# Optimization experiments

Hardware: AMD Instinct MI355X
Metric: run time of the kernel (lower is better)

## Reference

```python
import jax, jax.numpy as jnp
import numpy as np
import math

B, H, S, D = 2, 8, 2048, 64

def setup_inputs() -> dict:
    key = jax.random.key(0)
    kq, kk, kv = jax.random.split(key, 3)
    q = jax.random.normal(kq, (B, H, S, D), dtype=jnp.float32)
    k = jax.random.normal(kk, (B, H, S, D), dtype=jnp.float32)
    v = jax.random.normal(kv, (B, H, S, D), dtype=jnp.float32)
    # causal mask: True means masked (filled with -1e9), matching masked_fill
    mask = jnp.triu(jnp.ones((S, S), dtype=jnp.bool_), k=1)
    return {"q": q, "k": k, "v": v, "mask": mask}

def reference(q, k, v, mask) -> jnp.ndarray:
    d_model = q.shape[-1]
    # [..., s, t] scores
    att = jnp.einsum('bhsd,bhtd->bhst', q, k) / math.sqrt(d_model)
    if mask is not None:
        # broadcast mask over leading dims; True -> -1e9
        att = jnp.where(mask, jnp.float32(-1e9), att)
    # numerically stable softmax over last axis (matches manual Softmax)
    att = jax.nn.softmax(att, axis=-1)
    return jnp.einsum('bhst,bhtd->bhsd', att, v)
```

## Files before the change

kernel.cpp:

```cpp
#include <hip/hip_runtime.h>

typedef __bf16 bf16x8 __attribute__((ext_vector_type(8)));
typedef float  f32x16 __attribute__((ext_vector_type(16)));

constexpr int Sn  = 2048;
constexpr int Dh  = 64;
constexpr int QT  = 32;
constexpr int KVT = 32;
constexpr int NBH = 16;
constexpr int NT  = Sn / QT;
constexpr int NW  = 8;
constexpr int TSTR = 4 * 64 * 8;

constexpr float SCL = 0.125f * 1.44269504088896340736f;

constexpr size_t ELEMS  = (size_t)NBH * Sn * Dh;
constexpr size_t QB_OFF = 0;
constexpr size_t KP_OFF = ELEMS;
constexpr size_t VP_OFF = 2 * ELEMS;
constexpr size_t WS_NEED = 3 * ELEMS * 2;

__device__ inline bf16x8 cvt8(float4 a, float4 b, float s) {
  bf16x8 r;
  r[0] = (__bf16)(a.x * s); r[1] = (__bf16)(a.y * s);
  r[2] = (__bf16)(a.z * s); r[3] = (__bf16)(a.w * s);
  r[4] = (__bf16)(b.x * s); r[5] = (__bf16)(b.y * s);
  r[6] = (__bf16)(b.z * s); r[7] = (__bf16)(b.w * s);
  return r;
}

__global__ __launch_bounds__(256) void prep(
    const float* __restrict__ q, const float* __restrict__ k,
    const float* __restrict__ v, __bf16* __restrict__ ws)
{
  __shared__ float tl[KVT][Dh + 1];
  const int g    = blockIdx.x;
  const int tid  = threadIdx.x;
  const int wv   = tid >> 6;
  const int lane = tid & 63;
  const int hi   = lane >> 5;
  const int ln   = lane & 31;
  const size_t tbase = (size_t)g * (KVT * Dh);

  {
    const float* qp = q + tbase + (size_t)tid * 8;
    const float4 a = *(const float4*)qp;
    const float4 b = *(const float4*)(qp + 4);
    *(bf16x8*)(ws + QB_OFF + tbase + (size_t)tid * 8) = cvt8(a, b, SCL);
  }
  {
    const float* kp = k + tbase;
#pragma unroll
    for (int e = 0; e < 2; ++e) {
      const int i4  = tid + e * 256;
      const float4 x = *(const float4*)(kp + (size_t)i4 * 4);
      const int row = i4 >> 4, col = (i4 & 15) * 4;
      tl[row][col] = x.x; tl[row][col + 1] = x.y;
      tl[row][col + 2] = x.z; tl[row][col + 3] = x.w;
    }
  }
  __syncthreads();
  {
    bf16x8 r;
#pragma unroll
    for (int i = 0; i < 8; ++i) r[i] = (__bf16)tl[ln][16 * wv + 8 * hi + i];
    *(bf16x8*)(ws + KP_OFF + ((size_t)(g * 4 + wv) * 64 + lane) * 8) = r;
  }
  __syncthreads();
  {
    const float* vp = v + tbase;
#pragma unroll
    for (int e = 0; e < 2; ++e) {
      const int i4  = tid + e * 256;
      const float4 x = *(const float4*)(vp + (size_t)i4 * 4);
      const int row = i4 >> 4, col = (i4 & 15) * 4;
      tl[row][col] = x.x; tl[row][col + 1] = x.y;
      tl[row][col + 2] = x.z; tl[row][col + 3] = x.w;
    }
  }
  __syncthreads();
  {
    const int dt = wv >> 1, T = wv & 1;
    bf16x8 r;
#pragma unroll
    for (int i = 0; i < 8; ++i) {
      const int row = 16 * T + 4 * hi + (i & 3) + 8 * (i >> 2);
      r[i] = (__bf16)tl[row][32 * dt + ln];
    }
    *(bf16x8*)(ws + VP_OFF + ((size_t)(g * 4 + wv) * 64 + lane) * 8) = r;
  }
}

#define LOADKV(K0,K1,K2,K3,V0,V1,V2,V3,kt_) do {                         \
    const __bf16* kp_ = kpB + (size_t)(kt_) * TSTR + lane * 8;           \
    K0 = *(const bf16x8*)(kp_);                                          \
    K1 = *(const bf16x8*)(kp_ + 512);                                    \
    K2 = *(const bf16x8*)(kp_ + 1024);                                   \
    K3 = *(const bf16x8*)(kp_ + 1536);                                   \
    const __bf16* vp_ = vpB + (size_t)(kt_) * TSTR + lane * 8;           \
    V0 = *(const bf16x8*)(vp_);                                          \
    V1 = *(const bf16x8*)(vp_ + 512);                                    \
    V2 = *(const bf16x8*)(vp_ + 1024);                                   \
    V3 = *(const bf16x8*)(vp_ + 1536);                                   \
  } while (0)

#define COMPUTE(K0,K1,K2,K3,V0,V1,V2,V3,kt_) do {                        \
    f32x16 st0, st1;                                                     \
    _Pragma("unroll")                                                    \
    for (int i_ = 0; i_ < 16; ++i_) { st0[i_] = 0.f; st1[i_] = 0.f; }    \
    st0 = __builtin_amdgcn_mfma_f32_32x32x16_bf16(K0, qf[0], st0, 0, 0, 0);\
    st1 = __builtin_amdgcn_mfma_f32_32x32x16_bf16(K2, qf[2], st1, 0, 0, 0);\
    st0 = __builtin_amdgcn_mfma_f32_32x32x16_bf16(K1, qf[1], st0, 0, 0, 0);\
    st1 = __builtin_amdgcn_mfma_f32_32x32x16_bf16(K3, qf[3], st1, 0, 0, 0);\
    _Pragma("unroll")                                                    \
    for (int i_ = 0; i_ < 16; ++i_) st0[i_] += st1[i_];                  \
    if ((kt_) == tile) {                                                 \
      _Pragma("unroll")                                                  \
      for (int r_ = 0; r_ < 16; ++r_) {                                  \
        const int tl_ = (r_ & 3) + 8 * (r_ >> 2) + 4 * hi;               \
        if (tl_ > ln) st0[r_] = -1e30f;                                  \
      }                                                                  \
    }                                                                    \
    float p[16];                                                         \
    _Pragma("unroll")                                                    \
    for (int r_ = 0; r_ < 16; ++r_) p[r_] = __builtin_amdgcn_exp2f(st0[r_]); \
    bf16x8 pa0, pa1;                                                     \
    _Pragma("unroll")                                                    \
    for (int i_ = 0; i_ < 8; ++i_) { pa0[i_] = (__bf16)p[i_]; pa1[i_] = (__bf16)p[8 + i_]; } \
    o0 = __builtin_amdgcn_mfma_f32_32x32x16_bf16(pa0, V0, o0, 0, 0, 0);  \
    o1 = __builtin_amdgcn_mfma_f32_32x32x16_bf16(pa0, V2, o1, 0, 0, 0);  \
    ls = __builtin_amdgcn_mfma_f32_32x32x16_bf16(pa0, ONESV, ls, 0, 0, 0);\
    o0 = __builtin_amdgcn_mfma_f32_32x32x16_bf16(pa1, V1, o0, 0, 0, 0);  \
    o1 = __builtin_amdgcn_mfma_f32_32x32x16_bf16(pa1, V3, o1, 0, 0, 0);  \
    ls = __builtin_amdgcn_mfma_f32_32x32x16_bf16(pa1, ONESV, ls, 0, 0, 0);\
  } while (0)

__global__ __launch_bounds__(512) void attn_bf16(
    const __bf16* __restrict__ ws, float* __restrict__ og)
{
  __shared__ __bf16 ldsO[NW][QT][Dh];
  __shared__ float  ldsL[NW][QT];

  const int b    = blockIdx.x;
  const int bh   = b & 15;
  const int pr   = b >> 4;
  const int tid  = threadIdx.x;
  const int w    = tid >> 6;
  const int lane = tid & 63;
  const int hi   = lane >> 5;
  const int ln   = lane & 31;

  const __bf16* qB  = ws + QB_OFF + (size_t)bh * Sn * Dh;
  const __bf16* kpB = ws + KP_OFF + (size_t)bh * NT * TSTR;
  const __bf16* vpB = ws + VP_OFF + (size_t)bh * NT * TSTR;

  bf16x8 ONESV;
#pragma unroll
  for (int i = 0; i < 8; ++i) ONESV[i] = (__bf16)1.0f;

  for (int ph = 0; ph < 2; ++ph) {
    const int tile = ph ? (63 - pr) : pr;

    bf16x8 qf[4];
    {
      const __bf16* qp = qB + ((size_t)(tile * QT + ln)) * Dh + 8 * hi;
#pragma unroll
      for (int c = 0; c < 4; ++c) qf[c] = *(const bf16x8*)(qp + 16 * c);
    }

    f32x16 o0, o1, ls;
#pragma unroll
    for (int i = 0; i < 16; ++i) { o0[i] = 0.f; o1[i] = 0.f; ls[i] = 0.f; }

    bf16x8 kA0, kA1, kA2, kA3, vA0, vA1, vA2, vA3;
    bf16x8 kB0, kB1, kB2, kB3, vB0, vB1, vB2, vB3;

    int kt = w;
    bool tailA = true;
    if (kt <= tile) LOADKV(kA0,kA1,kA2,kA3,vA0,vA1,vA2,vA3, kt);
    while (kt + NW <= tile) {
      LOADKV(kB0,kB1,kB2,kB3,vB0,vB1,vB2,vB3, kt + NW);
      COMPUTE(kA0,kA1,kA2,kA3,vA0,vA1,vA2,vA3, kt);
      kt += NW;
      if (kt + NW <= tile) {
        LOADKV(kA0,kA1,kA2,kA3,vA0,vA1,vA2,vA3, kt + NW);
        COMPUTE(kB0,kB1,kB2,kB3,vB0,vB1,vB2,vB3, kt);
        kt += NW;
      } else {
        COMPUTE(kB0,kB1,kB2,kB3,vB0,vB1,vB2,vB3, kt);
        kt += NW;
        tailA = false;
      }
    }
    if (tailA && kt <= tile) COMPUTE(kA0,kA1,kA2,kA3,vA0,vA1,vA2,vA3, kt);

#pragma unroll
    for (int r = 0; r < 16; ++r) {
      const int rl = (r & 3) + 8 * (r >> 2) + 4 * hi;
      ldsO[w][rl][ln]      = (__bf16)o0[r];
      ldsO[w][rl][32 + ln] = (__bf16)o1[r];
      if (ln == 0) ldsL[w][rl] = ls[r];
    }
    __syncthreads();

#pragma unroll
    for (int e = 0; e < 4; ++e) {
      const int i   = e * 512 + tid;
      const int row = i >> 6;
      const int col = i & 63;
      float L = 0.f, o = 0.f;
#pragma unroll
      for (int wv = 0; wv < NW; ++wv) {
        L += ldsL[wv][row];
        o += (float)ldsO[wv][row][col];
      }
      og[((size_t)bh * Sn + tile * QT + row) * Dh + col] = o / L;
    }
    __syncthreads();
  }
}

__global__ __launch_bounds__(256) void attn_f32(
    const float* __restrict__ qg, const float* __restrict__ kg,
    const float* __restrict__ vg, float* __restrict__ og)
{
  __shared__ float ldsO[4][QT][Dh];
  __shared__ float ldsM[4][QT];
  __shared__ float ldsL[4][QT];

  const int g    = blockIdx.x;
  const int bh   = g >> 6;
  const int idx  = g & 63;
  const int tile = (idx & 1) ? (63 - (idx >> 1)) : (idx >> 1);
  const int w    = threadIdx.x >> 6;
  const int lane = threadIdx.x & 63;
  const int hi   = lane >> 5;
  const int ln   = lane & 31;

  const size_t base = (size_t)bh * Sn * Dh;
  const float* Q = qg + base;
  const float* K = kg + base;
  const float* V = vg + base;
  float*       O = og + base;
  const int srow = tile * QT + ln;

  bf16x8 qf[4];
  {
    const float* qp = Q + (size_t)srow * Dh + 8 * hi;
#pragma unroll
    for (int c = 0; c < 4; ++c) {
      const float4 x = *(const float4*)(qp + 16 * c);
      const float4 y = *(const float4*)(qp + 16 * c + 4);
      qf[c] = cvt8(x, y, 0.125f);
    }
  }
  f32x16 o0, o1;
#pragma unroll
  for (int i = 0; i < 16; ++i) { o0[i] = 0.f; o1[i] = 0.f; }
  float m = -1e30f, lsum = 0.f;

  for (int kt = w; kt <= tile; kt += 4) {
    const int t0 = kt * KVT;
    bf16x8 kf[4];
    const float* kp = K + (size_t)(t0 + ln) * Dh + 8 * hi;
#pragma unroll
    for (int c = 0; c < 4; ++c) {
      const float4 x = *(const float4*)(kp + 16 * c);
      const float4 y = *(const float4*)(kp + 16 * c + 4);
      kf[c] = cvt8(x, y, 1.0f);
    }
    f32x16 st;
#pragma unroll
    for (int i = 0; i < 16; ++i) st[i] = 0.f;
#pragma unroll
    for (int c = 0; c < 4; ++c)
      st = __builtin_amdgcn_mfma_f32_32x32x16_bf16(kf[c], qf[c], st, 0, 0, 0);
    if (kt == tile) {
#pragma unroll
      for (int r = 0; r < 16; ++r) {
        const int tl = (r & 3) + 8 * (r >> 2) + 4 * hi;
        if (tl > ln) st[r] = -1e30f;
      }
    }
    float tmax = st[0];
#pragma unroll
    for (int r = 1; r < 16; ++r) tmax = fmaxf(tmax, st[r]);
    tmax = fmaxf(tmax, __shfl_xor(tmax, 32));
    const float mnew = fmaxf(m, tmax);
    const bool  resc = __any(mnew > m);
    const float corr = __expf(m - mnew);
    m = mnew;
    float p[16];
    float psum = 0.f;
#pragma unroll
    for (int r = 0; r < 16; ++r) { p[r] = __expf(st[r] - mnew); psum += p[r]; }
    psum += __shfl_xor(psum, 32);
    lsum = lsum * corr + psum;
    if (resc) {
#pragma unroll
      for (int r = 0; r < 16; ++r) {
        const float cr = __shfl(corr, (r & 3) + 8 * (r >> 2) + 4 * hi);
        o0[r] *= cr; o1[r] *= cr;
      }
    }
    bf16x8 pa0, pa1;
#pragma unroll
    for (int i = 0; i < 8; ++i) { pa0[i] = (__bf16)p[i]; pa1[i] = (__bf16)p[8 + i]; }
#pragma unroll
    for (int T = 0; T < 2; ++T) {
      const int tb = t0 + 16 * T + 4 * hi;
      bf16x8 vb0, vb1;
#pragma unroll
      for (int j = 0; j < 4; ++j) {
        const float* vp  = V + (size_t)(tb + j) * Dh + ln;
        const float* vp2 = V + (size_t)(tb + 8 + j) * Dh + ln;
        vb0[j]     = (__bf16)vp[0];
        vb1[j]     = (__bf16)vp[32];
        vb0[4 + j] = (__bf16)vp2[0];
        vb1[4 + j] = (__bf16)vp2[32];
      }
      const bf16x8 pa = T ? pa1 : pa0;
      o0 = __builtin_amdgcn_mfma_f32_32x32x16_bf16(pa, vb0, o0, 0, 0, 0);
      o1 = __builtin_amdgcn_mfma_f32_32x32x16_bf16(pa, vb1, o1, 0, 0, 0);
    }
  }
#pragma unroll
  for (int r = 0; r < 16; ++r) {
    const int rl = (r & 3) + 8 * (r >> 2) + 4 * hi;
    ldsO[w][rl][ln]      = o0[r];
    ldsO[w][rl][32 + ln] = o1[r];
  }
  if (hi == 0) { ldsM[w][ln] = m; ldsL[w][ln] = lsum; }
  __syncthreads();
  const int tid = threadIdx.x;
#pragma unroll
  for (int e = 0; e < 8; ++e) {
    const int i   = e * 256 + tid;
    const int row = i >> 6;
    const int col = i & 63;
    const float m0 = ldsM[0][row], m1 = ldsM[1][row], m2 = ldsM[2][row], m3 = ldsM[3][row];
    const float M  = fmaxf(fmaxf(m0, m1), fmaxf(m2, m3));
    const float e0 = __expf(m0 - M), e1 = __expf(m1 - M), e2 = __expf(m2 - M), e3 = __expf(m3 - M);
    const float L  = ldsL[0][row] * e0 + ldsL[1][row] * e1 + ldsL[2][row] * e2 + ldsL[3][row] * e3;
    const float o  = ldsO[0][row][col] * e0 + ldsO[1][row][col] * e1
                   + ldsO[2][row][col] * e2 + ldsO[3][row][col] * e3;
    O[(size_t)(tile * QT + row) * Dh + col] = o / L;
  }
}

extern "C" void kernel_launch(void* const* d_in, const int* in_sizes, int n_in,
                              void* d_out, int out_size, void* d_ws, size_t ws_size,
                              hipStream_t stream) {
  const float* q = (const float*)d_in[0];
  const float* k = (const float*)d_in[1];
  const float* v = (const float*)d_in[2];
  float* out = (float*)d_out;
  if (ws_size >= WS_NEED) {
    prep<<<dim3(NBH * NT), dim3(256), 0, stream>>>(q, k, v, (__bf16*)d_ws);
    attn_bf16<<<dim3(NBH * NT / 2), dim3(512), 0, stream>>>((const __bf16*)d_ws, out);
  } else {
    attn_f32<<<dim3(1024), dim3(256), 0, stream>>>(q, k, v, out);
  }
}
```

Before: 36.62 us.

## Process two adjacent query tiles per block to reuse K/V loads

Each 256-thread block now handles two adjacent 32-row query tiles (64 rows), so every loaded K/V tile is used for two QK and PV products instead of one. The earlier scheme paired a short and a long tile in two sequential phases with 8 waves. The row-sum is now a scalar accumulated from the exp values plus a cross-half shuffle, replacing the ones-vector MFMA. Blocks are ordered longest-first to help load balance. This costs more registers per wave (two Q fragment sets, four accumulators) and gives fewer waves per block.

Result: slower. 39.45 us (+7.7%).

```diff
diff --git a/kernel.cpp b/kernel.cpp
--- a/kernel.cpp
+++ b/kernel.cpp
@@ -5,11 +5,10 @@
 
 constexpr int Sn  = 2048;
 constexpr int Dh  = 64;
-constexpr int QT  = 32;
 constexpr int KVT = 32;
 constexpr int NBH = 16;
-constexpr int NT  = Sn / QT;
-constexpr int NW  = 8;
+constexpr int NT  = Sn / KVT;
+constexpr int NW  = 4;
 constexpr int TSTR = 4 * 64 * 8;
 
 constexpr float SCL = 0.125f * 1.44269504088896340736f;
@@ -104,46 +103,71 @@
     V3 = *(const bf16x8*)(vp_ + 1536);                                   \
   } while (0)
 
-#define COMPUTE(K0,K1,K2,K3,V0,V1,V2,V3,kt_) do {                        \
-    f32x16 st0, st1;                                                     \
+#define QK_EXP(STQ, QF, PA0, PA1, LS, K0,K1,K2,K3, MASKED) do {          \
+    f32x16 STQ;                                                          \
     _Pragma("unroll")                                                    \
-    for (int i_ = 0; i_ < 16; ++i_) { st0[i_] = 0.f; st1[i_] = 0.f; }    \
-    st0 = __builtin_amdgcn_mfma_f32_32x32x16_bf16(K0, qf[0], st0, 0, 0, 0);\
-    st1 = __builtin_amdgcn_mfma_f32_32x32x16_bf16(K2, qf[2], st1, 0, 0, 0);\
-    st0 = __builtin_amdgcn_mfma_f32_32x32x16_bf16(K1, qf[1], st0, 0, 0, 0);\
-    st1 = __builtin_amdgcn_mfma_f32_32x32x16_bf16(K3, qf[3], st1, 0, 0, 0);\
-    _Pragma("unroll")                                                    \
-    for (int i_ = 0; i_ < 16; ++i_) st0[i_] += st1[i_];                  \
-    if ((kt_) == tile) {                                                 \
+    for (int i_ = 0; i_ < 16; ++i_) STQ[i_] = 0.f;                       \
+    STQ = __builtin_amdgcn_mfma_f32_32x32x16_bf16(K0, QF[0], STQ, 0, 0, 0);\
+    STQ = __builtin_amdgcn_mfma_f32_32x32x16_bf16(K1, QF[1], STQ, 0, 0, 0);\
+    STQ = __builtin_amdgcn_mfma_f32_32x32x16_bf16(K2, QF[2], STQ, 0, 0, 0);\
+    STQ = __builtin_amdgcn_mfma_f32_32x32x16_bf16(K3, QF[3], STQ, 0, 0, 0);\
+    if (MASKED) {                                                        \
       _Pragma("unroll")                                                  \
       for (int r_ = 0; r_ < 16; ++r_) {                                  \
         const int tl_ = (r_ & 3) + 8 * (r_ >> 2) + 4 * hi;               \
-        if (tl_ > ln) st0[r_] = -1e30f;                                  \
+        if (tl_ > ln) STQ[r_] = -1e30f;                                  \
       }                                                                  \
     }                                                                    \
-    float p[16];                                                         \
+    float p_[16];                                                        \
     _Pragma("unroll")                                                    \
-    for (int r_ = 0; r_ < 16; ++r_) p[r_] = __builtin_amdgcn_exp2f(st0[r_]); \
-    bf16x8 pa0, pa1;                                                     \
+    for (int r_ = 0; r_ < 16; ++r_) p_[r_] = __builtin_amdgcn_exp2f(STQ[r_]); \
+    float s0_ = (p_[0]+p_[1]) + (p_[2]+p_[3]),   s1_ = (p_[4]+p_[5]) + (p_[6]+p_[7]);   \
+    float s2_ = (p_[8]+p_[9]) + (p_[10]+p_[11]), s3_ = (p_[12]+p_[13]) + (p_[14]+p_[15]);\
+    LS += (s0_ + s1_) + (s2_ + s3_);                                     \
     _Pragma("unroll")                                                    \
-    for (int i_ = 0; i_ < 8; ++i_) { pa0[i_] = (__bf16)p[i_]; pa1[i_] = (__bf16)p[8 + i_]; } \
-    o0 = __builtin_amdgcn_mfma_f32_32x32x16_bf16(pa0, V0, o0, 0, 0, 0);  \
-    o1 = __builtin_amdgcn_mfma_f32_32x32x16_bf16(pa0, V2, o1, 0, 0, 0);  \
-    ls = __builtin_amdgcn_mfma_f32_32x32x16_bf16(pa0, ONESV, ls, 0, 0, 0);\
-    o0 = __builtin_amdgcn_mfma_f32_32x32x16_bf16(pa1, V1, o0, 0, 0, 0);  \
-    o1 = __builtin_amdgcn_mfma_f32_32x32x16_bf16(pa1, V3, o1, 0, 0, 0);  \
-    ls = __builtin_amdgcn_mfma_f32_32x32x16_bf16(pa1, ONESV, ls, 0, 0, 0);\
-  } while (0)
-
-__global__ __launch_bounds__(512) void attn_bf16(
+    for (int i_ = 0; i_ < 8; ++i_) { PA0[i_] = (__bf16)p_[i_]; PA1[i_] = (__bf16)p_[8 + i_]; } \
+  } while (0)
+
+#define PV2(PA0, PA1, OA, OB, V0,V1,V2,V3) do {                          \
+    OA = __builtin_amdgcn_mfma_f32_32x32x16_bf16(PA0, V0, OA, 0, 0, 0);  \
+    OB = __builtin_amdgcn_mfma_f32_32x32x16_bf16(PA0, V2, OB, 0, 0, 0);  \
+    OA = __builtin_amdgcn_mfma_f32_32x32x16_bf16(PA1, V1, OA, 0, 0, 0);  \
+    OB = __builtin_amdgcn_mfma_f32_32x32x16_bf16(PA1, V3, OB, 0, 0, 0);  \
+  } while (0)
+
+#define COMPUTE2(K0,K1,K2,K3,V0,V1,V2,V3) do {                           \
+    bf16x8 pa00, pa01, pa10, pa11;                                       \
+    QK_EXP(st0_, qf0, pa00, pa01, ls0, K0,K1,K2,K3, false);              \
+    QK_EXP(st1_, qf1, pa10, pa11, ls1, K0,K1,K2,K3, false);              \
+    PV2(pa00, pa01, o00, o01, V0,V1,V2,V3);                              \
+    PV2(pa10, pa11, o10, o11, V0,V1,V2,V3);                              \
+  } while (0)
+
+#define COMPUTE_D0(K0,K1,K2,K3,V0,V1,V2,V3) do {                         \
+    bf16x8 pa00, pa01, pa10, pa11;                                       \
+    QK_EXP(st0_, qf0, pa00, pa01, ls0, K0,K1,K2,K3, true);               \
+    QK_EXP(st1_, qf1, pa10, pa11, ls1, K0,K1,K2,K3, false);              \
+    PV2(pa00, pa01, o00, o01, V0,V1,V2,V3);                              \
+    PV2(pa10, pa11, o10, o11, V0,V1,V2,V3);                              \
+  } while (0)
+
+#define COMPUTE_D1(K0,K1,K2,K3,V0,V1,V2,V3) do {                         \
+    bf16x8 pa10, pa11;                                                   \
+    QK_EXP(st1_, qf1, pa10, pa11, ls1, K0,K1,K2,K3, true);               \
+    PV2(pa10, pa11, o10, o11, V0,V1,V2,V3);                              \
+  } while (0)
+
+__global__ __launch_bounds__(256) void attn_bf16(
     const __bf16* __restrict__ ws, float* __restrict__ og)
 {
-  __shared__ __bf16 ldsO[NW][QT][Dh];
-  __shared__ float  ldsL[NW][QT];
+  __shared__ __bf16 ldsO[NW][64][Dh];
+  __shared__ float  ldsL[NW][64];
 
   const int b    = blockIdx.x;
-  const int bh   = b & 15;
-  const int pr   = b >> 4;
+  const int bb   = b & 255;
+  const int bh   = 2 * (bb & 7) + ((bb >> 3) & 1);
+  const int p    = (b < 256) ? (31 - (bb >> 4)) : (bb >> 4);
+  const int t0   = 2 * p, t1 = 2 * p + 1;
   const int tid  = threadIdx.x;
   const int w    = tid >> 6;
   const int lane = tid & 63;
@@ -154,69 +178,72 @@
   const __bf16* kpB = ws + KP_OFF + (size_t)bh * NT * TSTR;
   const __bf16* vpB = ws + VP_OFF + (size_t)bh * NT * TSTR;
 
-  bf16x8 ONESV;
-#pragma unroll
-  for (int i = 0; i < 8; ++i) ONESV[i] = (__bf16)1.0f;
-
-  for (int ph = 0; ph < 2; ++ph) {
-    const int tile = ph ? (63 - pr) : pr;
-
-    bf16x8 qf[4];
-    {
-      const __bf16* qp = qB + ((size_t)(tile * QT + ln)) * Dh + 8 * hi;
-#pragma unroll
-      for (int c = 0; c < 4; ++c) qf[c] = *(const bf16x8*)(qp + 16 * c);
-    }
-
-    f32x16 o0, o1, ls;
-#pragma unroll
-    for (int i = 0; i < 16; ++i) { o0[i] = 0.f; o1[i] = 0.f; ls[i] = 0.f; }
-
-    bf16x8 kA0, kA1, kA2, kA3, vA0, vA1, vA2, vA3;
-    bf16x8 kB0, kB1, kB2, kB3, vB0, vB1, vB2, vB3;
-
-    int kt = w;
-    bool tailA = true;
-    if (kt <= tile) LOADKV(kA0,kA1,kA2,kA3,vA0,vA1,vA2,vA3, kt);
-    while (kt + NW <= tile) {
-      LOADKV(kB0,kB1,kB2,kB3,vB0,vB1,vB2,vB3, kt + NW);
-      COMPUTE(kA0,kA1,kA2,kA3,vA0,vA1,vA2,vA3, kt);
-      kt += NW;
-      if (kt + NW <= tile) {
-        LOADKV(kA0,kA1,kA2,kA3,vA0,vA1,vA2,vA3, kt + NW);
-        COMPUTE(kB0,kB1,kB2,kB3,vB0,vB1,vB2,vB3, kt);
-        kt += NW;
-      } else {
-        COMPUTE(kB0,kB1,kB2,kB3,vB0,vB1,vB2,vB3, kt);
-        kt += NW;
-        tailA = false;
-      }
-    }
-    if (tailA && kt <= tile) COMPUTE(kA0,kA1,kA2,kA3,vA0,vA1,vA2,vA3, kt);
-
-#pragma unroll
-    for (int r = 0; r < 16; ++r) {
-      const int rl = (r & 3) + 8 * (r >> 2) + 4 * hi;
-      ldsO[w][rl][ln]      = (__bf16)o0[r];
-      ldsO[w][rl][32 + ln] = (__bf16)o1[r];
-      if (ln == 0) ldsL[w][rl] = ls[r];
-    }
-    __syncthreads();
-
-#pragma unroll
-    for (int e = 0; e < 4; ++e) {
-      const int i   = e * 512 + tid;
-      const int row = i >> 6;
-      const int col = i & 63;
-      float L = 0.f, o = 0.f;
-#pragma unroll
-      for (int wv = 0; wv < NW; ++wv) {
-        L += ldsL[wv][row];
-        o += (float)ldsO[wv][row][col];
-      }
-      og[((size_t)bh * Sn + tile * QT + row) * Dh + col] = o / L;
-    }
-    __syncthreads();
+  bf16x8 qf0[4], qf1[4];
+  {
+    const __bf16* qp0 = qB + ((size_t)(t0 * 32 + ln)) * Dh + 8 * hi;
+    const __bf16* qp1 = qB + ((size_t)(t1 * 32 + ln)) * Dh + 8 * hi;
+#pragma unroll
+    for (int c = 0; c < 4; ++c) {
+      qf0[c] = *(const bf16x8*)(qp0 + 16 * c);
+      qf1[c] = *(const bf16x8*)(qp1 + 16 * c);
+    }
+  }
+
+  f32x16 o00, o01, o10, o11;
+#pragma unroll
+  for (int i = 0; i < 16; ++i) { o00[i] = 0.f; o01[i] = 0.f; o10[i] = 0.f; o11[i] = 0.f; }
+  float ls0 = 0.f, ls1 = 0.f;
+
+  bf16x8 kA0, kA1, kA2, kA3, vA0, vA1, vA2, vA3;
+  bf16x8 kB0, kB1, kB2, kB3, vB0, vB1, vB2, vB3;
+
+  int kt = w;
+  while (kt + NW < t0) {
+    LOADKV(kA0,kA1,kA2,kA3,vA0,vA1,vA2,vA3, kt);
+    LOADKV(kB0,kB1,kB2,kB3,vB0,vB1,vB2,vB3, kt + NW);
+    COMPUTE2(kA0,kA1,kA2,kA3,vA0,vA1,vA2,vA3);
+    COMPUTE2(kB0,kB1,kB2,kB3,vB0,vB1,vB2,vB3);
+    kt += 2 * NW;
+  }
+  if (kt < t0) {
+    LOADKV(kA0,kA1,kA2,kA3,vA0,vA1,vA2,vA3, kt);
+    COMPUTE2(kA0,kA1,kA2,kA3,vA0,vA1,vA2,vA3);
+  }
+  if ((t0 & (NW - 1)) == w) {
+    LOADKV(kA0,kA1,kA2,kA3,vA0,vA1,vA2,vA3, t0);
+    COMPUTE_D0(kA0,kA1,kA2,kA3,vA0,vA1,vA2,vA3);
+  }
+  if ((t1 & (NW - 1)) == w) {
+    LOADKV(kA0,kA1,kA2,kA3,vA0,vA1,vA2,vA3, t1);
+    COMPUTE_D1(kA0,kA1,kA2,kA3,vA0,vA1,vA2,vA3);
+  }
+
+  ls0 += __shfl_xor(ls0, 32);
+  ls1 += __shfl_xor(ls1, 32);
+
+#pragma unroll
+  for (int r = 0; r < 16; ++r) {
+    const int rl = (r & 3) + 8 * (r >> 2) + 4 * hi;
+    ldsO[w][rl][ln]           = (__bf16)o00[r];
+    ldsO[w][rl][32 + ln]      = (__bf16)o01[r];
+    ldsO[w][32 + rl][ln]      = (__bf16)o10[r];
+    ldsO[w][32 + rl][32 + ln] = (__bf16)o11[r];
+  }
+  if (hi == 0) { ldsL[w][ln] = ls0; ldsL[w][32 + ln] = ls1; }
+  __syncthreads();
+
+#pragma unroll
+  for (int e = 0; e < 16; ++e) {
+    const int i   = e * 256 + tid;
+    const int row = i >> 6;
+    const int col = i & 63;
+    float L = 0.f, o = 0.f;
+#pragma unroll
+    for (int wv = 0; wv < NW; ++wv) {
+      L += ldsL[wv][row];
+      o += (float)ldsO[wv][row][col];
+    }
+    og[((size_t)bh * Sn + p * 64 + row) * Dh + col] = o / L;
   }
 }
 
@@ -224,9 +251,9 @@
     const float* __restrict__ qg, const float* __restrict__ kg,
     const float* __restrict__ vg, float* __restrict__ og)
 {
-  __shared__ float ldsO[4][QT][Dh];
-  __shared__ float ldsM[4][QT];
-  __shared__ float ldsL[4][QT];
+  __shared__ float ldsO[4][32][Dh];
+  __shared__ float ldsM[4][32];
+  __shared__ float ldsL[4][32];
 
   const int g    = blockIdx.x;
   const int bh   = g >> 6;
@@ -242,7 +269,7 @@
   const float* K = kg + base;
   const float* V = vg + base;
   float*       O = og + base;
-  const int srow = tile * QT + ln;
+  const int srow = tile * 32 + ln;
 
   bf16x8 qf[4];
   {
@@ -260,7 +287,7 @@
   float m = -1e30f, lsum = 0.f;
 
   for (int kt = w; kt <= tile; kt += 4) {
-    const int t0 = kt * KVT;
+    const int t0 = kt * 32;
     bf16x8 kf[4];
     const float* kp = K + (size_t)(t0 + ln) * Dh + 8 * hi;
 #pragma unroll
@@ -344,7 +371,7 @@
     const float L  = ldsL[0][row] * e0 + ldsL[1][row] * e1 + ldsL[2][row] * e2 + ldsL[3][row] * e3;
     const float o  = ldsO[0][row][col] * e0 + ldsO[1][row][col] * e1
                    + ldsO[2][row][col] * e2 + ldsO[3][row][col] * e3;
-    O[(size_t)(tile * QT + row) * Dh + col] = o / L;
+    O[(size_t)(tile * 32 + row) * Dh + col] = o / L;
   }
 }
 
@@ -357,7 +384,7 @@
   float* out = (float*)d_out;
   if (ws_size >= WS_NEED) {
     prep<<<dim3(NBH * NT), dim3(256), 0, stream>>>(q, k, v, (__bf16*)d_ws);
-    attn_bf16<<<dim3(NBH * NT / 2), dim3(512), 0, stream>>>((const __bf16*)d_ws, out);
+    attn_bf16<<<dim3(NBH * NT / 2), dim3(256), 0, stream>>>((const __bf16*)d_ws, out);
   } else {
     attn_f32<<<dim3(1024), dim3(256), 0, stream>>>(q, k, v, out);
   }
```
